# Performance work log

Measured on AMD Instinct MI355X. Metric: run time of the kernel, lower is better.

## Reference

```python
import jax, jax.numpy as jnp
import numpy as np

B, T, D = 1, 2048, 2048
H, HD = 32, 64
HEAD_COUNTS = np.array([8, 6, 4, 4, 6, 4])  # reasoning, creativity, curiosity, emotional, memory, meta
NEG = -1e9


def rope_tables(seq_len, dim, dtype):
    inv_freq = 1.0 / (10000.0 ** (jnp.arange(0, dim, 2, dtype=jnp.float32) / dim))
    t = jnp.arange(seq_len, dtype=jnp.float32)
    freqs = jnp.outer(t, inv_freq)            # [T, dim/2]
    emb = jnp.concatenate([freqs, freqs], -1) # [T, dim]
    return jnp.cos(emb).astype(dtype), jnp.sin(emb).astype(dtype)


def rotate_half(x):
    x1, x2 = jnp.split(x, 2, axis=-1)
    return jnp.concatenate([-x2, x1], axis=-1)


def setup_inputs() -> dict:
    key = jax.random.key(0)
    ks = jax.random.split(key, 8)
    x = jax.random.normal(ks[0], (B, T, D), jnp.float32)
    mask = jnp.tril(jnp.ones((T, T), jnp.int32))[None, None]  # causal [1,1,T,T]
    context_bias = jax.random.normal(ks[1], (B, T, T), jnp.float32) * 0.02
    mod_weights = jax.random.uniform(ks[2], (B, 6), jnp.float32, 0.5, 1.5)
    Wq = jax.random.normal(ks[3], (D, D), jnp.float32) * 0.02
    Wk = jax.random.normal(ks[4], (D, D), jnp.float32) * 0.02
    Wv = jax.random.normal(ks[5], (D, D), jnp.float32) * 0.02
    Wo = jax.random.normal(ks[6], (D, D), jnp.float32) * 0.02
    temp_scales = jnp.ones((H,), jnp.float32)
    return {"x": x, "mask": mask, "context_bias": context_bias,
            "mod_weights": mod_weights, "Wq": Wq, "Wk": Wk, "Wv": Wv,
            "Wo": Wo, "temp_scales": temp_scales}


def reference(x, mask, context_bias, mod_weights, Wq, Wk, Wv, Wo, temp_scales):
    b, t, d = x.shape
    # projections (torch Linear: y = x @ W.T)
    Q = (x @ Wq.T).reshape(b, t, H, HD).transpose(0, 2, 1, 3)  # [B,H,T,HD]
    K = (x @ Wk.T).reshape(b, t, H, HD).transpose(0, 2, 1, 3)
    V = (x @ Wv.T).reshape(b, t, H, HD).transpose(0, 2, 1, 3)
    cos, sin = rope_tables(t, HD, x.dtype)
    cos, sin = cos[None, None], sin[None, None]
    Q = Q * cos + rotate_half(Q) * sin
    K = K * cos + rotate_half(K) * sin
    scale = (HD ** -0.5) * temp_scales.reshape(1, H, 1, 1)
    attn = jnp.einsum('bhqd,bhkd->bhqk', Q, K) * scale
    attn = jnp.where(mask == 0, NEG, attn)
    attn = attn + context_bias[:, None]
    # per-head module reweight: expand [B,6] -> [B,H]
    w = jnp.repeat(mod_weights, np.asarray(HEAD_COUNTS), axis=1, total_repeat_length=H)
    attn = attn * w[:, :, None, None]
    attn = jax.nn.softmax(attn, axis=-1)
    out = jnp.einsum('bhqk,bhkd->bhqd', attn, V)
    out = out.transpose(0, 2, 1, 3).reshape(b, t, d)
    return out @ Wo.T
```

## Files before the change

### kernel.cpp

```cpp
#include <hip/hip_runtime.h>
#include <hip/hip_bf16.h>
#include <cstdint>
#include <cstddef>

typedef __bf16 bf16;
typedef bf16 bf16x8 __attribute__((ext_vector_type(8)));
typedef float f32x4 __attribute__((ext_vector_type(4)));

#define MFMA_BF16(a,b,c) __builtin_amdgcn_mfma_f32_16x16x32_bf16((a),(b),(c),0,0,0)

typedef __attribute__((address_space(1))) const void gvoid;
typedef __attribute__((address_space(3))) void svoid;
__device__ __forceinline__ void gload16(const bf16* g, bf16* l){
  __builtin_amdgcn_global_load_lds((gvoid*)g, (svoid*)l, 16, 0, 0);
}

__device__ __forceinline__ int head_group(int h){
  return (h<8)?0:(h<14)?1:(h<18)?2:(h<22)?3:(h<28)?4:5;
}

struct CvtArgs { const float* src[6]; bf16* dst[6]; };
__global__ __launch_bounds__(256) void cvt6_kernel(CvtArgs a, int n){
  const int z = blockIdx.y;
  const float* __restrict__ in = a.src[z];
  bf16* __restrict__ out = a.dst[z];
  int i = (blockIdx.x*256 + threadIdx.x)*8;
  if (i >= n) return;
  const float4* p = (const float4*)(in + i);
  float4 va = p[0], vb = p[1];
  bf16x8 o;
  o[0]=(bf16)va.x; o[1]=(bf16)va.y; o[2]=(bf16)va.z; o[3]=(bf16)va.w;
  o[4]=(bf16)vb.x; o[5]=(bf16)vb.y; o[6]=(bf16)vb.z; o[7]=(bf16)vb.w;
  *(bf16x8*)(out+i) = o;
}

__global__ void rope_tab_kernel(float* __restrict__ cosT, float* __restrict__ sinT){
  int t = blockIdx.x, i = threadIdx.x;
  float invf = powf(10000.0f, -((float)i)/32.0f);
  float ang = (float)t * invf;
  cosT[t*32+i] = cosf(ang);
  sinT[t*32+i] = sinf(ang);
}

template<bool F32OUT>
__device__ __forceinline__ void gemm_body(const bf16* __restrict__ A,
                                          const bf16* __restrict__ B,
                                          void* __restrict__ Cv){
  __shared__ bf16 As[128*32];
  __shared__ bf16 Bs[128*32];
  const int tid  = threadIdx.x;
  const int wave = tid>>6, lane = tid&63;
  const int l16  = lane&15, lg = lane>>4;
  const int wr   = wave>>1, wc = wave&1;
  const int row0 = blockIdx.y*128, col0 = blockIdx.x*128;

  const bf16* Ag0 = A + (size_t)(row0 + wave*32      + (lane>>2))*2048 + (lane&3)*8;
  const bf16* Ag1 = A + (size_t)(row0 + wave*32 + 16 + (lane>>2))*2048 + (lane&3)*8;
  const bf16* Bg0 = B + (size_t)(col0 + wave*32      + (lane>>2))*2048 + (lane&3)*8;
  const bf16* Bg1 = B + (size_t)(col0 + wave*32 + 16 + (lane>>2))*2048 + (lane&3)*8;
  bf16* AsB0 = As + (wave*32     )*32;
  bf16* AsB1 = As + (wave*32 + 16)*32;
  bf16* BsB0 = Bs + (wave*32     )*32;
  bf16* BsB1 = Bs + (wave*32 + 16)*32;

  f32x4 acc[4][4];
  #pragma unroll
  for (int m=0;m<4;++m)
    #pragma unroll
    for (int n=0;n<4;++n)
      #pragma unroll
      for (int r=0;r<4;++r) acc[m][n][r] = 0.f;

  for (int kt=0; kt<64; ++kt){
    const int ko = kt*32;
    gload16(Ag0 + ko, AsB0);
    gload16(Ag1 + ko, AsB1);
    gload16(Bg0 + ko, BsB0);
    gload16(Bg1 + ko, BsB1);
    __syncthreads();
    bf16x8 af[4], bfr[4];
    #pragma unroll
    for (int m=0;m<4;++m) af[m]  = *(const bf16x8*)&As[(wr*64+m*16+l16)*32 + lg*8];
    #pragma unroll
    for (int n=0;n<4;++n) bfr[n] = *(const bf16x8*)&Bs[(wc*64+n*16+l16)*32 + lg*8];
    #pragma unroll
    for (int m=0;m<4;++m)
      #pragma unroll
      for (int n=0;n<4;++n)
        acc[m][n] = MFMA_BF16(af[m], bfr[n], acc[m][n]);
    __syncthreads();
  }

  #pragma unroll
  for (int m=0;m<4;++m)
    #pragma unroll
    for (int n=0;n<4;++n)
      #pragma unroll
      for (int r=0;r<4;++r){
        size_t idx = (size_t)(row0 + wr*64 + m*16 + lg*4 + r)*2048
                   + col0 + wc*64 + n*16 + l16;
        if constexpr (F32OUT) ((float*)Cv)[idx] = acc[m][n][r];
        else                  ((bf16*)Cv)[idx]  = (bf16)acc[m][n][r];
      }
}

__global__ __launch_bounds__(256) void gemm_qkv_kernel(
    const bf16* __restrict__ A,
    const bf16* __restrict__ B0, const bf16* __restrict__ B1, const bf16* __restrict__ B2,
    bf16* __restrict__ C0, bf16* __restrict__ C1, bf16* __restrict__ C2){
  const bf16* B = (blockIdx.z==0)?B0:((blockIdx.z==1)?B1:B2);
  bf16*       C = (blockIdx.z==0)?C0:((blockIdx.z==1)?C1:C2);
  gemm_body<false>(A, B, C);
}

__global__ __launch_bounds__(256) void gemm_out_kernel(
    const bf16* __restrict__ A, const bf16* __restrict__ B, float* __restrict__ C){
  gemm_body<true>(A, B, C);
}

__global__ __launch_bounds__(512) void rope_apply_kernel(
    const bf16* __restrict__ Qr, const bf16* __restrict__ Kr,
    const float* __restrict__ cosT, const float* __restrict__ sinT,
    const float* __restrict__ mw, const float* __restrict__ ts,
    bf16* __restrict__ Qs, bf16* __restrict__ Ks){
  const int t = blockIdx.x;
  const int tid = threadIdx.x;
  const int h = tid>>4, j = tid&15;
  const float sc = 0.125f * ts[h] * mw[head_group(h)];
  const size_t ib = (size_t)t*2048 + h*64;
  const size_t ob = ((size_t)h*2048 + t)*64;
  #pragma unroll
  for (int u=0; u<2; ++u){
    const int i = j*2 + u;
    const float c = cosT[t*32+i], s = sinT[t*32+i];
    const float q1 = (float)Qr[ib+i], q2 = (float)Qr[ib+32+i];
    Qs[ob+i]    = (bf16)((q1*c - q2*s)*sc);
    Qs[ob+32+i] = (bf16)((q2*c + q1*s)*sc);
    const float k1 = (float)Kr[ib+i], k2 = (float)Kr[ib+32+i];
    Ks[ob+i]    = (bf16)(k1*c - k2*s);
    Ks[ob+32+i] = (bf16)(k2*c + k1*s);
  }
}

__global__ __launch_bounds__(256) void vtrans_kernel(const bf16* __restrict__ V,
                                                     bf16* __restrict__ Vt){
  __shared__ bf16 lds[64][72];
  const int tb = blockIdx.x, h = blockIdx.y;
  const int tid = threadIdx.x;
  {
    const int r = tid>>2, c0 = (tid&3)*16;
    const bf16* src = V + (size_t)(tb*64 + r)*2048 + h*64 + c0;
    bf16x8 v0 = *(const bf16x8*)src;
    bf16x8 v1 = *(const bf16x8*)(src+8);
    *(bf16x8*)&lds[r][c0]   = v0;
    *(bf16x8*)&lds[r][c0+8] = v1;
  }
  __syncthreads();
  {
    const int d = tid>>2, t0 = (tid&3)*16;
    bf16x8 o0, o1;
    #pragma unroll
    for (int jj=0;jj<8;++jj){ o0[jj] = lds[t0+jj][d]; o1[jj] = lds[t0+8+jj][d]; }
    bf16* dst = Vt + (size_t)(h*64 + d)*2048 + tb*64 + t0;
    *(bf16x8*)dst     = o0;
    *(bf16x8*)(dst+8) = o1;
  }
}

__global__ __launch_bounds__(512) void attn_kernel(
    const bf16* __restrict__ Qs, const bf16* __restrict__ Ks,
    const bf16* __restrict__ Vt, const bf16* __restrict__ biasb,
    const float* __restrict__ mw, bf16* __restrict__ attout){
  const int n  = blockIdx.x;
  const int h  = ((n>>8)<<4) | ((n>>4)&15);
  const int qt = (n&256) ? (n&15) : 15-(n&15);
  const int tid = threadIdx.x, wid = tid>>6, lane = tid&63;
  const int l16 = lane&15, lg = lane>>4;
  const float w_h = mw[head_group(h)];
  const int qbase = qt*128 + wid*16;
  const int qg0 = qbase + lg*4;
  const int qtop = qbase + 15;
  const int nkt = 2*qt + 2;

  __shared__ bf16 Kl[2][4096];
  __shared__ bf16 Vl[2][4096];
  __shared__ bf16 plds[8][16][72];

  const int srow = tid>>3, ssub = tid&7;
  const bf16* Kg = Ks + (size_t)h*2048*64 + srow*64 + ssub*8;
  const bf16* Vg = Vt + ((size_t)h*64 + srow)*2048 + ssub*8;
  const int wsw = srow*64 + ((ssub ^ (srow&7))<<3);

  const bf16* Qp = Qs + ((size_t)h*2048 + qbase + l16)*64 + lg*8;
  bf16x8 qf0 = *(const bf16x8*)Qp;
  bf16x8 qf1 = *(const bf16x8*)(Qp + 32);

  const bf16* Bg = biasb + (size_t)qg0*2048;

  f32x4 O[4];
  float l[4] = {0.f,0.f,0.f,0.f};
  #pragma unroll
  for (int c=0;c<4;++c)
    #pragma unroll
    for (int r=0;r<4;++r) O[c][r] = 0.f;

  int rK0[4], rK1[4];
  #pragma unroll
  for (int c=0;c<4;++c){
    const int row = c*16 + l16;
    rK0[c] = row*64 + (((lg  ) ^ (row&7))<<3);
    rK1[c] = row*64 + (((4+lg) ^ (row&7))<<3);
  }

  {
    bf16x8 k0v = *(const bf16x8*)Kg;
    bf16x8 v0v = *(const bf16x8*)Vg;
    *(bf16x8*)&Kl[0][wsw] = k0v;
    *(bf16x8*)&Vl[0][wsw] = v0v;
  }
  __syncthreads();

  int cur = 0;
  for (int kt=0; kt<nkt; ++kt){
    const int k0 = kt*64;
    const bool more = (kt+1 < nkt);
    bf16x8 kA, vA;
    if (more){
      kA = *(const bf16x8*)(Kg + (size_t)(k0+64)*64);
      vA = *(const bf16x8*)(Vg + (k0+64));
    }

    if (k0 <= qtop){
      float bv[4][4];
      #pragma unroll
      for (int c=0;c<4;++c)
        #pragma unroll
        for (int r=0;r<4;++r)
          bv[c][r] = (float)Bg[(size_t)r*2048 + k0 + c*16 + l16];

      f32x4 S[4];
      #pragma unroll
      for (int c=0;c<4;++c)
        #pragma unroll
        for (int r=0;r<4;++r) S[c][r] = 0.f;
      #pragma unroll
      for (int c=0;c<4;++c){
        bf16x8 kf0 = *(const bf16x8*)&Kl[cur][rK0[c]];
        bf16x8 kf1 = *(const bf16x8*)&Kl[cur][rK1[c]];
        S[c] = MFMA_BF16(qf0, kf0, S[c]);
        S[c] = MFMA_BF16(qf1, kf1, S[c]);
      }

      #pragma unroll
      for (int c=0;c<4;++c){
        const int kg = k0 + c*16 + l16;
        #pragma unroll
        for (int r=0;r<4;++r){
          float s = S[c][r] + w_h*bv[c][r];
          if (kg > qg0+r) s = -1e30f;
          const float p = __expf(s - 4.0f);
          S[c][r] = p; l[r] += p;
        }
      }

      #pragma unroll
      for (int c=0;c<4;++c)
        #pragma unroll
        for (int r=0;r<4;++r)
          plds[wid][lg*4+r][c*16+l16] = (bf16)S[c][r];
      bf16x8 pf0 = *(const bf16x8*)&plds[wid][l16][lg*8];
      bf16x8 pf1 = *(const bf16x8*)&plds[wid][l16][lg*8+32];

      #pragma unroll
      for (int c=0;c<4;++c){
        bf16x8 vf0 = *(const bf16x8*)&Vl[cur][rK0[c]];
        bf16x8 vf1 = *(const bf16x8*)&Vl[cur][rK1[c]];
        O[c] = MFMA_BF16(pf0, vf0, O[c]);
        O[c] = MFMA_BF16(pf1, vf1, O[c]);
      }
    }

    if (more){
      *(bf16x8*)&Kl[cur^1][wsw] = kA;
      *(bf16x8*)&Vl[cur^1][wsw] = vA;
    }
    __syncthreads();
    cur ^= (int)more;
  }

  #pragma unroll
  for (int r=0;r<4;++r){
    float v = l[r];
    v += __shfl_xor(v,1);
    v += __shfl_xor(v,2);
    v += __shfl_xor(v,4);
    v += __shfl_xor(v,8);
    l[r] = 1.0f / v;
  }
  #pragma unroll
  for (int c=0;c<4;++c)
    #pragma unroll
    for (int r=0;r<4;++r)
      attout[(size_t)(qg0+r)*2048 + h*64 + c*16 + l16] = (bf16)(O[c][r]*l[r]);
}

extern "C" void kernel_launch(void* const* d_in, const int* in_sizes, int n_in,
                              void* d_out, int out_size, void* d_ws, size_t ws_size,
                              hipStream_t stream){
  const float* x    = (const float*)d_in[0];
  const float* bias = (const float*)d_in[2];
  const float* mw   = (const float*)d_in[3];
  const float* Wq   = (const float*)d_in[4];
  const float* Wk   = (const float*)d_in[5];
  const float* Wv   = (const float*)d_in[6];
  const float* Wo   = (const float*)d_in[7];
  const float* ts   = (const float*)d_in[8];
  float* out = (float*)d_out;

  const size_t SZ = (size_t)2048*2048;
  bf16* base = (bf16*)d_ws;
  bf16* xb   = base;
  bf16* Wqb  = base + 1*SZ;
  bf16* Wkb  = base + 2*SZ;
  bf16* Wvb  = base + 3*SZ;
  bf16* Wob  = base + 4*SZ;
  bf16* bb   = base + 5*SZ;
  bf16* Qraw = base + 6*SZ;
  bf16* Kraw = base + 7*SZ;
  bf16* Vraw = base + 8*SZ;
  bf16* Qsb  = base + 9*SZ;
  bf16* Ksb  = base + 10*SZ;
  bf16* Vtb  = base + 11*SZ;
  float* cosT = (float*)(base + 12*SZ);
  float* sinT = cosT + 2048*32;
  bf16* att = Qraw;

  CvtArgs ca;
  ca.src[0]=x;  ca.src[1]=bias; ca.src[2]=Wq;  ca.src[3]=Wk;  ca.src[4]=Wv;  ca.src[5]=Wo;
  ca.dst[0]=xb; ca.dst[1]=bb;   ca.dst[2]=Wqb; ca.dst[3]=Wkb; ca.dst[4]=Wvb; ca.dst[5]=Wob;
  const int nb = (int)(SZ/8/256);
  cvt6_kernel<<<dim3(nb,6),256,0,stream>>>(ca, (int)SZ);
  rope_tab_kernel<<<2048,32,0,stream>>>(cosT, sinT);
  gemm_qkv_kernel<<<dim3(16,16,3),256,0,stream>>>(xb, Wqb,Wkb,Wvb, Qraw,Kraw,Vraw);
  rope_apply_kernel<<<2048,512,0,stream>>>(Qraw,Kraw,cosT,sinT,mw,ts,Qsb,Ksb);
  vtrans_kernel<<<dim3(32,32),256,0,stream>>>(Vraw, Vtb);
  attn_kernel<<<512,512,0,stream>>>(Qsb,Ksb,Vtb,bb,mw,att);
  gemm_out_kernel<<<dim3(16,16),256,0,stream>>>(att, Wob, out);
}
```

Before: 198.2 us.

## Fuse RoPE and V transpose into QKV GEMM epilogue; read fp32 bias directly

The QKV projection GEMM now applies RoPE plus Q scaling in its epilogue and writes Q/K straight into head-major layout, and writes V directly transposed. This removes the separate rope_apply and vtrans kernels and their intermediate round trips through global memory. The context bias is no longer converted to bf16; the attention kernel reads the fp32 bias directly, which saves one conversion pass but doubles the bias bytes read inside attention. The epilogue stores are scalar and strided, so store efficiency may drop.

```diff
diff --git a/kernel.cpp b/kernel.cpp
--- a/kernel.cpp
+++ b/kernel.cpp
@@ -4,6 +4,7 @@
 #include <cstddef>
 
 typedef __bf16 bf16;
+typedef bf16 bf16x4 __attribute__((ext_vector_type(4)));
 typedef bf16 bf16x8 __attribute__((ext_vector_type(8)));
 typedef float f32x4 __attribute__((ext_vector_type(4)));
 
@@ -19,8 +20,8 @@
   return (h<8)?0:(h<14)?1:(h<18)?2:(h<22)?3:(h<28)?4:5;
 }
 
-struct CvtArgs { const float* src[6]; bf16* dst[6]; };
-__global__ __launch_bounds__(256) void cvt6_kernel(CvtArgs a, int n){
+struct CvtArgs { const float* src[5]; bf16* dst[5]; };
+__global__ __launch_bounds__(256) void cvt5_kernel(CvtArgs a, int n){
   const int z = blockIdx.y;
   const float* __restrict__ in = a.src[z];
   bf16* __restrict__ out = a.dst[z];
@@ -42,17 +43,16 @@
   sinT[t*32+i] = sinf(ang);
 }
 
-template<bool F32OUT>
-__device__ __forceinline__ void gemm_body(const bf16* __restrict__ A,
+__device__ __forceinline__ void gemm_core(const bf16* __restrict__ A,
                                           const bf16* __restrict__ B,
-                                          void* __restrict__ Cv){
+                                          int row0, int col0,
+                                          f32x4 (&acc)[4][4]){
   __shared__ bf16 As[128*32];
   __shared__ bf16 Bs[128*32];
   const int tid  = threadIdx.x;
   const int wave = tid>>6, lane = tid&63;
   const int l16  = lane&15, lg = lane>>4;
   const int wr   = wave>>1, wc = wave&1;
-  const int row0 = blockIdx.y*128, col0 = blockIdx.x*128;
 
   const bf16* Ag0 = A + (size_t)(row0 + wave*32      + (lane>>2))*2048 + (lane&3)*8;
   const bf16* Ag1 = A + (size_t)(row0 + wave*32 + 16 + (lane>>2))*2048 + (lane&3)*8;
@@ -63,7 +63,6 @@
   bf16* BsB0 = Bs + (wave*32     )*32;
   bf16* BsB1 = Bs + (wave*32 + 16)*32;
 
-  f32x4 acc[4][4];
   #pragma unroll
   for (int m=0;m<4;++m)
     #pragma unroll
@@ -90,7 +89,73 @@
         acc[m][n] = MFMA_BF16(af[m], bfr[n], acc[m][n]);
     __syncthreads();
   }
-
+}
+
+__global__ __launch_bounds__(256) void gemm_qkv_kernel(
+    const bf16* __restrict__ A,
+    const bf16* __restrict__ B0, const bf16* __restrict__ B1, const bf16* __restrict__ B2,
+    bf16* __restrict__ Qs, bf16* __restrict__ Ks, bf16* __restrict__ Vt,
+    const float* __restrict__ cosT, const float* __restrict__ sinT,
+    const float* __restrict__ mw, const float* __restrict__ ts){
+  const int z = blockIdx.z;
+  const bf16* B = (z==0)?B0:((z==1)?B1:B2);
+  const int row0 = blockIdx.y*128, col0 = blockIdx.x*128;
+
+  f32x4 acc[4][4];
+  gemm_core(A, B, row0, col0, acc);
+
+  const int tid  = threadIdx.x;
+  const int wave = tid>>6, lane = tid&63;
+  const int l16  = lane&15, lg = lane>>4;
+  const int wr   = wave>>1, wc = wave&1;
+  const int h    = (col0 + wc*64) >> 6;
+
+  if (z == 2){
+    #pragma unroll
+    for (int n=0;n<4;++n){
+      const int d = n*16 + l16;
+      #pragma unroll
+      for (int m=0;m<4;++m){
+        const int t0 = row0 + wr*64 + m*16 + lg*4;
+        bf16x4 v;
+        #pragma unroll
+        for (int r=0;r<4;++r) v[r] = (bf16)acc[m][n][r];
+        *(bf16x4*)&Vt[((size_t)h*64 + d)*2048 + t0] = v;
+      }
+    }
+  } else {
+    const float sc = (z==0) ? 0.125f*ts[h]*mw[head_group(h)] : 1.0f;
+    bf16* Out = (z==0) ? Qs : Ks;
+    #pragma unroll
+    for (int m=0;m<4;++m){
+      #pragma unroll
+      for (int r=0;r<4;++r){
+        const int t = row0 + wr*64 + m*16 + lg*4 + r;
+        const float* ct = cosT + t*32;
+        const float* st = sinT + t*32;
+        bf16* dst = Out + ((size_t)h*2048 + t)*64;
+        #pragma unroll
+        for (int n=0;n<2;++n){
+          const int i = n*16 + l16;
+          const float c = ct[i], s = st[i];
+          const float a1 = acc[m][n][r], a2 = acc[m][n+2][r];
+          dst[i]    = (bf16)((a1*c - a2*s)*sc);
+          dst[i+32] = (bf16)((a2*c + a1*s)*sc);
+        }
+      }
+    }
+  }
+}
+
+__global__ __launch_bounds__(256) void gemm_out_kernel(
+    const bf16* __restrict__ A, const bf16* __restrict__ B, float* __restrict__ C){
+  const int row0 = blockIdx.y*128, col0 = blockIdx.x*128;
+  f32x4 acc[4][4];
+  gemm_core(A, B, row0, col0, acc);
+  const int tid  = threadIdx.x;
+  const int wave = tid>>6, lane = tid&63;
+  const int l16  = lane&15, lg = lane>>4;
+  const int wr   = wave>>1, wc = wave&1;
   #pragma unroll
   for (int m=0;m<4;++m)
     #pragma unroll
@@ -99,77 +164,13 @@
       for (int r=0;r<4;++r){
         size_t idx = (size_t)(row0 + wr*64 + m*16 + lg*4 + r)*2048
                    + col0 + wc*64 + n*16 + l16;
-        if constexpr (F32OUT) ((float*)Cv)[idx] = acc[m][n][r];
-        else                  ((bf16*)Cv)[idx]  = (bf16)acc[m][n][r];
-      }
-}
-
-__global__ __launch_bounds__(256) void gemm_qkv_kernel(
-    const bf16* __restrict__ A,
-    const bf16* __restrict__ B0, const bf16* __restrict__ B1, const bf16* __restrict__ B2,
-    bf16* __restrict__ C0, bf16* __restrict__ C1, bf16* __restrict__ C2){
-  const bf16* B = (blockIdx.z==0)?B0:((blockIdx.z==1)?B1:B2);
-  bf16*       C = (blockIdx.z==0)?C0:((blockIdx.z==1)?C1:C2);
-  gemm_body<false>(A, B, C);
-}
-
-__global__ __launch_bounds__(256) void gemm_out_kernel(
-    const bf16* __restrict__ A, const bf16* __restrict__ B, float* __restrict__ C){
-  gemm_body<true>(A, B, C);
-}
-
-__global__ __launch_bounds__(512) void rope_apply_kernel(
-    const bf16* __restrict__ Qr, const bf16* __restrict__ Kr,
-    const float* __restrict__ cosT, const float* __restrict__ sinT,
-    const float* __restrict__ mw, const float* __restrict__ ts,
-    bf16* __restrict__ Qs, bf16* __restrict__ Ks){
-  const int t = blockIdx.x;
-  const int tid = threadIdx.x;
-  const int h = tid>>4, j = tid&15;
-  const float sc = 0.125f * ts[h] * mw[head_group(h)];
-  const size_t ib = (size_t)t*2048 + h*64;
-  const size_t ob = ((size_t)h*2048 + t)*64;
-  #pragma unroll
-  for (int u=0; u<2; ++u){
-    const int i = j*2 + u;
-    const float c = cosT[t*32+i], s = sinT[t*32+i];
-    const float q1 = (float)Qr[ib+i], q2 = (float)Qr[ib+32+i];
-    Qs[ob+i]    = (bf16)((q1*c - q2*s)*sc);
-    Qs[ob+32+i] = (bf16)((q2*c + q1*s)*sc);
-    const float k1 = (float)Kr[ib+i], k2 = (float)Kr[ib+32+i];
-    Ks[ob+i]    = (bf16)(k1*c - k2*s);
-    Ks[ob+32+i] = (bf16)(k2*c + k1*s);
-  }
-}
-
-__global__ __launch_bounds__(256) void vtrans_kernel(const bf16* __restrict__ V,
-                                                     bf16* __restrict__ Vt){
-  __shared__ bf16 lds[64][72];
-  const int tb = blockIdx.x, h = blockIdx.y;
-  const int tid = threadIdx.x;
-  {
-    const int r = tid>>2, c0 = (tid&3)*16;
-    const bf16* src = V + (size_t)(tb*64 + r)*2048 + h*64 + c0;
-    bf16x8 v0 = *(const bf16x8*)src;
-    bf16x8 v1 = *(const bf16x8*)(src+8);
-    *(bf16x8*)&lds[r][c0]   = v0;
-    *(bf16x8*)&lds[r][c0+8] = v1;
-  }
-  __syncthreads();
-  {
-    const int d = tid>>2, t0 = (tid&3)*16;
-    bf16x8 o0, o1;
-    #pragma unroll
-    for (int jj=0;jj<8;++jj){ o0[jj] = lds[t0+jj][d]; o1[jj] = lds[t0+8+jj][d]; }
-    bf16* dst = Vt + (size_t)(h*64 + d)*2048 + tb*64 + t0;
-    *(bf16x8*)dst     = o0;
-    *(bf16x8*)(dst+8) = o1;
-  }
+        C[idx] = acc[m][n][r];
+      }
 }
 
 __global__ __launch_bounds__(512) void attn_kernel(
     const bf16* __restrict__ Qs, const bf16* __restrict__ Ks,
-    const bf16* __restrict__ Vt, const bf16* __restrict__ biasb,
+    const bf16* __restrict__ Vt, const float* __restrict__ biasf,
     const float* __restrict__ mw, bf16* __restrict__ attout){
   const int n  = blockIdx.x;
   const int h  = ((n>>8)<<4) | ((n>>4)&15);
@@ -195,7 +196,7 @@
   bf16x8 qf0 = *(const bf16x8*)Qp;
   bf16x8 qf1 = *(const bf16x8*)(Qp + 32);
 
-  const bf16* Bg = biasb + (size_t)qg0*2048;
+  const float* Bg = biasf + (size_t)qg0*2048;
 
   f32x4 O[4];
   float l[4] = {0.f,0.f,0.f,0.f};
@@ -236,7 +237,7 @@
       for (int c=0;c<4;++c)
         #pragma unroll
         for (int r=0;r<4;++r)
-          bv[c][r] = (float)Bg[(size_t)r*2048 + k0 + c*16 + l16];
+          bv[c][r] = Bg[(size_t)r*2048 + k0 + c*16 + l16];
 
       f32x4 S[4];
       #pragma unroll
@@ -324,26 +325,21 @@
   bf16* Wkb  = base + 2*SZ;
   bf16* Wvb  = base + 3*SZ;
   bf16* Wob  = base + 4*SZ;
-  bf16* bb   = base + 5*SZ;
-  bf16* Qraw = base + 6*SZ;
-  bf16* Kraw = base + 7*SZ;
-  bf16* Vraw = base + 8*SZ;
-  bf16* Qsb  = base + 9*SZ;
-  bf16* Ksb  = base + 10*SZ;
-  bf16* Vtb  = base + 11*SZ;
-  float* cosT = (float*)(base + 12*SZ);
+  bf16* Qsb  = base + 5*SZ;
+  bf16* Ksb  = base + 6*SZ;
+  bf16* Vtb  = base + 7*SZ;
+  bf16* att  = base + 8*SZ;
+  float* cosT = (float*)(base + 9*SZ);
   float* sinT = cosT + 2048*32;
-  bf16* att = Qraw;
 
   CvtArgs ca;
-  ca.src[0]=x;  ca.src[1]=bias; ca.src[2]=Wq;  ca.src[3]=Wk;  ca.src[4]=Wv;  ca.src[5]=Wo;
-  ca.dst[0]=xb; ca.dst[1]=bb;   ca.dst[2]=Wqb; ca.dst[3]=Wkb; ca.dst[4]=Wvb; ca.dst[5]=Wob;
+  ca.src[0]=x;  ca.src[1]=Wq;  ca.src[2]=Wk;  ca.src[3]=Wv;  ca.src[4]=Wo;
+  ca.dst[0]=xb; ca.dst[1]=Wqb; ca.dst[2]=Wkb; ca.dst[3]=Wvb; ca.dst[4]=Wob;
   const int nb = (int)(SZ/8/256);
-  cvt6_kernel<<<dim3(nb,6),256,0,stream>>>(ca, (int)SZ);
+  cvt5_kernel<<<dim3(nb,5),256,0,stream>>>(ca, (int)SZ);
   rope_tab_kernel<<<2048,32,0,stream>>>(cosT, sinT);
-  gemm_qkv_kernel<<<dim3(16,16,3),256,0,stream>>>(xb, Wqb,Wkb,Wvb, Qraw,Kraw,Vraw);
-  rope_apply_kernel<<<2048,512,0,stream>>>(Qraw,Kraw,cosT,sinT,mw,ts,Qsb,Ksb);
-  vtrans_kernel<<<dim3(32,32),256,0,stream>>>(Vraw, Vtb);
-  attn_kernel<<<512,512,0,stream>>>(Qsb,Ksb,Vtb,bb,mw,att);
+  gemm_qkv_kernel<<<dim3(16,16,3),256,0,stream>>>(xb, Wqb,Wkb,Wvb,
+                                                  Qsb,Ksb,Vtb, cosT,sinT, mw,ts);
+  attn_kernel<<<512,512,0,stream>>>(Qsb,Ksb,Vtb,bias,mw,att);
   gemm_out_kernel<<<dim3(16,16),256,0,stream>>>(att, Wob, out);
 }
```

Result: faster. 181.6 us (-8.4%).
